# Optimization experiments

Measured on AMD Instinct MI355X. Metric: run time of the kernel, lower is better.

The kernel has to match this reference:

```python
import jax, jax.numpy as jnp
import numpy as np


def setup_inputs() -> dict:
    key = jax.random.key(0)
    k1, k2, k3, k4, k5 = jax.random.split(key, 5)
    in_f, out_f, rank = 4096, 4096, 16
    std = 1.0 / np.sqrt(rank)
    x = jax.random.normal(k1, (4, 2048, in_f), dtype=jnp.float32)
    base_weight = jax.random.normal(k2, (out_f, in_f), dtype=jnp.float32) * 0.02
    lora_A = jax.random.normal(k3, (rank, in_f), dtype=jnp.float32) * std
    lora_B = jax.random.normal(k4, (out_f, rank), dtype=jnp.float32) * 0.01
    magnitude_vec = jax.random.uniform(k5, (out_f,), dtype=jnp.float32) + 0.5
    return {"x": x, "base_weight": base_weight, "lora_A": lora_A,
            "lora_B": lora_B, "magnitude_vec": magnitude_vec}


def reference(x, base_weight, lora_A, lora_B, magnitude_vec):
    # x: [B, S, in] -> tokens [N, in]
    out_shape = (*x.shape[:-1], base_weight.shape[0])
    xt = x.reshape(-1, x.shape[-1])
    # low-rank adapter path: [N, rank] @ [rank, out]
    lora_out = (xt @ lora_A.T) @ lora_B.T
    # column-wise L2 norm of adapted weight, per output row: [out]
    adapted_w = base_weight + lora_B @ lora_A
    column_norm = jnp.linalg.norm(adapted_w, axis=1)
    magnitude_scale = magnitude_vec / column_norm  # [out]
    # base GEMM + adapter + magnitude rescale epilogue
    dora_out = (xt @ base_weight.T + lora_out) * magnitude_scale[None, :]
    return dora_out.reshape(out_shape)
```

## Files before the change

kernel.cpp:

```cpp
#include <hip/hip_runtime.h>
#include <hip/hip_bf16.h>
#include <stdint.h>

typedef __attribute__((ext_vector_type(8))) short s16x8;
typedef __attribute__((ext_vector_type(4))) float f32x4;
typedef __attribute__((ext_vector_type(4))) unsigned short us4;

__device__ inline unsigned short bf_rne(float f) {
    union { float f; uint32_t u; } v; v.f = f;
    uint32_t u = v.u;
    u += 0x7FFFu + ((u >> 16) & 1u);
    return (unsigned short)(u >> 16);
}

#define GLD_LDS16(gp, lp)                                                     \
    __builtin_amdgcn_global_load_lds(                                         \
        (const __attribute__((address_space(1))) void*)(gp),                  \
        (__attribute__((address_space(3))) void*)(lp), 16, 0, 0)

#define LDSOFF(p) ((unsigned)(uintptr_t)(__attribute__((address_space(3))) const void*)(p))

__global__ __launch_bounds__(256) void prologue_kernel(
    const float4* __restrict__ x4, us4* __restrict__ xbf4,
    const float4* __restrict__ W4,
    const float4* __restrict__ A4,
    const float* __restrict__ B,
    const float* __restrict__ mag,
    unsigned short* __restrict__ wbf,
    float* __restrict__ scale) {
    const int tid = threadIdx.x;
    if (blockIdx.x < 512) {
        const int m0 = blockIdx.x * 8;
        __shared__ float Bs[8][16];
        __shared__ float red[32];
        if (tid < 128) Bs[tid >> 4][tid & 15] = B[m0 * 16 + tid];
        __syncthreads();
        float ss[8] = {};
        for (int c = tid; c < 1024; c += 256) {
            float4 a[16];
#pragma unroll
            for (int r = 0; r < 16; ++r) a[r] = A4[r * 1024 + c];
#pragma unroll
            for (int i = 0; i < 8; ++i) {
                float4 w = W4[(size_t)(m0 + i) * 1024 + c];
#pragma unroll
                for (int r = 0; r < 16; ++r) {
                    const float br = Bs[i][r];
                    w.x += br * a[r].x; w.y += br * a[r].y;
                    w.z += br * a[r].z; w.w += br * a[r].w;
                }
                ss[i] += w.x * w.x + w.y * w.y + w.z * w.z + w.w * w.w;
                us4 o; o[0] = bf_rne(w.x); o[1] = bf_rne(w.y);
                o[2] = bf_rne(w.z); o[3] = bf_rne(w.w);
                *(us4*)&wbf[(size_t)(m0 + i) * 4096 + c * 4] = o;
            }
        }
        const int lane = tid & 63, wv = tid >> 6;
#pragma unroll
        for (int i = 0; i < 8; ++i) {
            float v = ss[i];
#pragma unroll
            for (int off = 32; off > 0; off >>= 1) v += __shfl_down(v, off, 64);
            if (lane == 0) red[wv * 8 + i] = v;
        }
        __syncthreads();
        if (tid < 8) {
            float tot = red[tid] + red[8 + tid] + red[16 + tid] + red[24 + tid];
            scale[m0 + tid] = mag[m0 + tid] / sqrtf(tot);
        }
    } else {
        const size_t base = (size_t)(blockIdx.x - 512) * 1024 + tid;
#pragma unroll
        for (int j = 0; j < 4; ++j) {
            const size_t idx = base + j * 256;
            float4 a = x4[idx];
            us4 o;
            o[0] = bf_rne(a.x); o[1] = bf_rne(a.y);
            o[2] = bf_rne(a.z); o[3] = bf_rne(a.w);
            xbf4[idx] = o;
        }
    }
}

#define FENCE() asm volatile("" ::: "memory")
#define BAR()   do { FENCE(); __builtin_amdgcn_s_barrier(); FENCE(); } while (0)
#define VMW(n)  asm volatile("s_waitcnt vmcnt(" #n ")" ::: "memory")
#define LGW(n)  asm volatile("s_waitcnt lgkmcnt(" #n ")" ::: "memory")
#define SB0()   __builtin_amdgcn_sched_barrier(0)
#define PRIO1() __builtin_amdgcn_s_setprio(1)
#define PRIO0() __builtin_amdgcn_s_setprio(0)

#define DSR(dst, va, IMM) \
    asm volatile("ds_read_b128 %0, %1 offset:" #IMM : "=v"(dst) : "v"(va))

__global__ __launch_bounds__(512, 2) void dora_gemm(
    const unsigned short* __restrict__ xbf,
    const unsigned short* __restrict__ wbf,
    const float* __restrict__ scale,
    float* __restrict__ out) {
    __shared__ __align__(16) unsigned short As[2][256 * 64];
    __shared__ __align__(16) unsigned short Bs[2][256 * 64];

    const int tid  = threadIdx.x;
    const int lane = tid & 63;
    const int w    = tid >> 6;
    const int wm   = w >> 2;
    const int wn   = w & 3;
    const int q    = lane >> 4;
    const int c15  = lane & 15;

    const int bid = blockIdx.x;
    const int xcd = bid & 7, sub = bid >> 3;
    const int tileM = (((xcd & 3) << 3) | (sub & 7)) << 8;
    const int tileN = (((xcd >> 2) << 3) | (sub >> 3)) << 8;

    const int r0 = tid >> 3;
    const int lc = (tid & 7) ^ (r0 & 7);
    const size_t aoff = (size_t)(tileM + r0) * 4096 + lc * 8;
    const size_t boff = (size_t)(tileN + r0) * 4096 + lc * 8;
    const int ld0 = (w * 64) * 8;
    const int ld1 = (512 + w * 64) * 8;

#define STAGE_A(d, h, k0) do {                                                            \
    GLD_LDS16(xbf + aoff + (size_t)((h) * 128) * 4096 + (k0),      &As[d][(h) * 8192 + ld0]); \
    GLD_LDS16(xbf + aoff + (size_t)((h) * 128 + 64) * 4096 + (k0), &As[d][(h) * 8192 + ld1]); \
} while (0)
#define STAGE_B(d, h, k0) do {                                                            \
    GLD_LDS16(wbf + boff + (size_t)((h) * 128) * 4096 + (k0),      &Bs[d][(h) * 8192 + ld0]); \
    GLD_LDS16(wbf + boff + (size_t)((h) * 128 + 64) * 4096 + (k0), &Bs[d][(h) * 8192 + ld1]); \
} while (0)

    const int rb = c15 & 7;
    unsigned aA[4][2], aB[2][2];
#pragma unroll
    for (int mt = 0; mt < 4; ++mt)
#pragma unroll
        for (int kc = 0; kc < 2; ++kc)
            aA[mt][kc] = LDSOFF(&As[0][(wm * 64 + mt * 16 + c15) * 64 +
                                       ((kc * 4 + q) ^ rb) * 8]);
#pragma unroll
    for (int nt = 0; nt < 2; ++nt)
#pragma unroll
        for (int kc = 0; kc < 2; ++kc)
            aB[nt][kc] = LDSOFF(&Bs[0][(wn * 32 + nt * 16 + c15) * 64 +
                                       ((kc * 4 + q) ^ rb) * 8]);

    s16x8 af[4][2];
    s16x8 bfx[2][2][2];
    f32x4 acc[8][4] = {};

#define RD_A(IMM) do {                                                        \
    DSR(af[0][0], aA[0][0], IMM); DSR(af[0][1], aA[0][1], IMM);               \
    DSR(af[1][0], aA[1][0], IMM); DSR(af[1][1], aA[1][1], IMM);               \
    DSR(af[2][0], aA[2][0], IMM); DSR(af[2][1], aA[2][1], IMM);               \
    DSR(af[3][0], aA[3][0], IMM); DSR(af[3][1], aA[3][1], IMM); } while (0)
#define RD_B(nh, IMM) do {                                                    \
    DSR(bfx[nh][0][0], aB[0][0], IMM); DSR(bfx[nh][0][1], aB[0][1], IMM);     \
    DSR(bfx[nh][1][0], aB[1][0], IMM); DSR(bfx[nh][1][1], aB[1][1], IMM); } while (0)

#define MFMA_Q(mh, nh) do {                                                   \
    _Pragma("unroll") for (int mt = 0; mt < 4; ++mt)                          \
    _Pragma("unroll") for (int nt = 0; nt < 2; ++nt)                          \
    _Pragma("unroll") for (int kc = 0; kc < 2; ++kc)                          \
        acc[(mh) * 4 + mt][(nh) * 2 + nt] =                                   \
            __builtin_amdgcn_mfma_f32_16x16x32_bf16(                          \
                af[mt][kc], bfx[nh][nt][kc],                                  \
                acc[(mh) * 4 + mt][(nh) * 2 + nt], 0, 0, 0);                  \
} while (0)

#define TILE1(IA0, IA1, IB0, IB1, DD, KN) do {                                \
    VMW(0); BAR();                                                            \
    STAGE_A(DD, 0, KN); STAGE_B(DD, 0, KN);                                   \
    STAGE_B(DD, 1, KN); STAGE_A(DD, 1, KN);                                   \
    RD_B(0, IB0); RD_A(IA0);                                                  \
    RD_B(1, IB1);                                                             \
    LGW(4); SB0(); PRIO1(); MFMA_Q(0, 0); PRIO0();                            \
    LGW(0); SB0(); PRIO1(); MFMA_Q(0, 1); PRIO0();                            \
    RD_A(IA1);                                                                \
    LGW(0); SB0(); PRIO1(); MFMA_Q(1, 1); PRIO0();                            \
    PRIO1(); MFMA_Q(1, 0); PRIO0();                                           \
} while (0)

    STAGE_A(0, 0, 0); STAGE_B(0, 0, 0); STAGE_B(0, 1, 0); STAGE_A(0, 1, 0);

    for (int kn = 64; kn <= 3904; kn += 128) {
        TILE1(0, 16384, 0, 16384, 1, kn);
        TILE1(32768, 49152, 32768, 49152, 0, kn + 64);
    }
    TILE1(0, 16384, 0, 16384, 1, 4032);
    VMW(0); BAR();
    RD_B(0, 32768); RD_A(32768);
    RD_B(1, 49152);
    LGW(4); SB0(); PRIO1(); MFMA_Q(0, 0); PRIO0();
    LGW(0); SB0(); PRIO1(); MFMA_Q(0, 1); PRIO0();
    RD_A(49152);
    LGW(0); SB0(); PRIO1(); MFMA_Q(1, 1); MFMA_Q(1, 0); PRIO0();

#pragma unroll
    for (int nh = 0; nh < 2; ++nh)
#pragma unroll
    for (int nt = 0; nt < 2; ++nt) {
        const int col = tileN + nh * 128 + wn * 32 + nt * 16 + c15;
        const float s = scale[col];
#pragma unroll
        for (int mh = 0; mh < 2; ++mh)
#pragma unroll
        for (int mt = 0; mt < 4; ++mt) {
            const int row0 = tileM + mh * 128 + wm * 64 + mt * 16 + q * 4;
#pragma unroll
            for (int r = 0; r < 4; ++r)
                out[(size_t)(row0 + r) * 4096 + col] = acc[mh * 4 + mt][nh * 2 + nt][r] * s;
        }
    }
}

extern "C" void kernel_launch(void* const* d_in, const int* in_sizes, int n_in,
                              void* d_out, int out_size, void* d_ws, size_t ws_size,
                              hipStream_t stream) {
    const float* x   = (const float*)d_in[0];
    const float* W   = (const float*)d_in[1];
    const float* A   = (const float*)d_in[2];
    const float* B   = (const float*)d_in[3];
    const float* mag = (const float*)d_in[4];
    float* out = (float*)d_out;

    const size_t XBF_BYTES = (size_t)8192 * 4096 * 2;
    const size_t WBF_BYTES = (size_t)4096 * 4096 * 2;
    const size_t NEEDED = XBF_BYTES + WBF_BYTES + 4096 * sizeof(float);
    if (ws_size < NEEDED) return;

    unsigned short* xbf = (unsigned short*)d_ws;
    unsigned short* wbf = (unsigned short*)((char*)d_ws + XBF_BYTES);
    float* scale = (float*)((char*)d_ws + XBF_BYTES + WBF_BYTES);

    prologue_kernel<<<8704, 256, 0, stream>>>((const float4*)x, (us4*)xbf,
                                              (const float4*)W, (const float4*)A,
                                              B, mag, wbf, scale);
    dora_gemm<<<512, 512, 0, stream>>>(xbf, wbf, scale, out);
}
```

Before: 313.9 us.

## Restructure GEMM main loop into barrier-split ping-pong schedule with prefetched fragments

```diff
diff --git a/kernel.cpp b/kernel.cpp
--- a/kernel.cpp
+++ b/kernel.cpp
@@ -168,33 +168,46 @@
                 acc[(mh) * 4 + mt][(nh) * 2 + nt], 0, 0, 0);                  \
 } while (0)
 
-#define TILE1(IA0, IA1, IB0, IB1, DD, KN) do {                                \
-    VMW(0); BAR();                                                            \
+#define TILE(IB1, IA1, IAN, IBN, DD, KN) do {                                 \
+                                                       \
+    LGW(0); SB0();                                                            \
     STAGE_A(DD, 0, KN); STAGE_B(DD, 0, KN);                                   \
     STAGE_B(DD, 1, KN); STAGE_A(DD, 1, KN);                                   \
-    RD_B(0, IB0); RD_A(IA0);                                                  \
+    PRIO1(); MFMA_Q(0, 0); PRIO0();                                           \
     RD_B(1, IB1);                                                             \
-    LGW(4); SB0(); PRIO1(); MFMA_Q(0, 0); PRIO0();                            \
-    LGW(0); SB0(); PRIO1(); MFMA_Q(0, 1); PRIO0();                            \
+    BAR();                                                                    \
+                                                       \
+    LGW(0); SB0();                                                            \
+    PRIO1(); MFMA_Q(0, 1); PRIO0();                                           \
     RD_A(IA1);                                                                \
-    LGW(0); SB0(); PRIO1(); MFMA_Q(1, 1); PRIO0();                            \
+    BAR();                                                                    \
+            \
+    LGW(0); SB0();                                                            \
+    PRIO1(); MFMA_Q(1, 1); PRIO0();                                           \
+    VMW(0); BAR();                                                            \
+        \
     PRIO1(); MFMA_Q(1, 0); PRIO0();                                           \
+    RD_A(IAN); RD_B(0, IBN);                                                  \
+    BAR();                                                                    \
 } while (0)
 
     STAGE_A(0, 0, 0); STAGE_B(0, 0, 0); STAGE_B(0, 1, 0); STAGE_A(0, 1, 0);
+    VMW(0); BAR();
+    RD_A(0); RD_B(0, 0);
 
     for (int kn = 64; kn <= 3904; kn += 128) {
-        TILE1(0, 16384, 0, 16384, 1, kn);
-        TILE1(32768, 49152, 32768, 49152, 0, kn + 64);
+        TILE(16384, 16384, 32768, 32768, 1, kn);
+        TILE(49152, 49152, 0, 0, 0, kn + 64);
     }
-    TILE1(0, 16384, 0, 16384, 1, 4032);
-    VMW(0); BAR();
-    RD_B(0, 32768); RD_A(32768);
+    TILE(16384, 16384, 32768, 32768, 1, 4032);
+    LGW(0); SB0();
+    PRIO1(); MFMA_Q(0, 0); PRIO0();
     RD_B(1, 49152);
-    LGW(4); SB0(); PRIO1(); MFMA_Q(0, 0); PRIO0();
-    LGW(0); SB0(); PRIO1(); MFMA_Q(0, 1); PRIO0();
+    LGW(0); SB0();
+    PRIO1(); MFMA_Q(0, 1); PRIO0();
     RD_A(49152);
-    LGW(0); SB0(); PRIO1(); MFMA_Q(1, 1); MFMA_Q(1, 0); PRIO0();
+    LGW(0); SB0();
+    PRIO1(); MFMA_Q(1, 1); MFMA_Q(1, 0); PRIO0();
 
 #pragma unroll
     for (int nh = 0; nh < 2; ++nh)
```

Measured after the change: 322.7 us. 1.03x slower.
